# Kernel optimization log

Hardware: AMD Instinct MI355X
Metric: run time of the kernel (lower is better)

## Reference

```python
import jax, jax.numpy as jnp
import numpy as np

D = 256            # voxel grid resolution per axis
B, H, N = 1, 480 * 640, 9   # batch, pixels, samples per ray


def setup_inputs() -> dict:
    key = jax.random.key(0)
    k1, k2, k3 = jax.random.split(key, 3)
    # ray sample points in voxel coordinates; range slightly exceeds the grid
    # so the out-of-bounds masking path is exercised.
    points = jax.random.uniform(k1, (B, H, N, 3), dtype=jnp.float32,
                                minval=-2.0, maxval=float(D) + 1.0)
    tsdf_volume = jax.random.normal(k2, (D, D, D), dtype=jnp.float32)
    weights_volume = jax.random.uniform(k3, (D, D, D), dtype=jnp.float32)
    return {"points": points, "tsdf_volume": tsdf_volume,
            "weights_volume": weights_volume}


# binary corner offsets in the same (i, j, k) loop order as the original
_OFFS = np.array([[(c >> 2) & 1, (c >> 1) & 1, c & 1] for c in range(8)],
                 dtype=np.float32)  # [8, 3]


def _trilinear(points, tsdf_volume, weights_volume):
    b, h, n, _ = points.shape
    p = points.reshape(-1, 3)                      # [M, 3]
    idx = jnp.floor(p)
    center = idx + 0.5                             # mode='center'
    neighbor = jnp.sign(center - p)                # +-1 (0 exactly at center)
    alpha = jnp.abs(p - center)                    # [M, 3]
    alpha_inv = 1.0 - alpha
    offs = jnp.asarray(_OFFS, dtype=p.dtype)       # [8, 3]
    # per-corner trilinear weight: prod over dims of (alpha_inv if off==0 else alpha)
    w = jnp.prod(jnp.where(offs[None] == 0,
                           alpha_inv[:, None, :], alpha[:, None, :]),
                 axis=-1)                          # [M, 8]
    corner = idx[:, None, :] + offs[None] * neighbor[:, None, :]  # [M, 8, 3]
    ci = corner.astype(jnp.int32)
    dims = jnp.asarray(tsdf_volume.shape, dtype=jnp.int32)
    valid = jnp.all((ci >= 0) & (ci < dims[None, None, :]), axis=-1)  # [M, 8]
    cc = jnp.clip(ci, 0, dims[None, None, :] - 1)
    vmask = valid.astype(p.dtype)
    tv = tsdf_volume[cc[..., 0], cc[..., 1], cc[..., 2]] * vmask      # [M, 8]
    wv = weights_volume[cc[..., 0], cc[..., 1], cc[..., 2]] * vmask   # [M, 8]
    fusion_values = jnp.sum(tv * w, axis=1).reshape(b, h, n)
    fusion_weights = jnp.sum(wv * w, axis=1).reshape(b, h, n)
    indices = ci.reshape(b, h, n, 8, 3)
    weights = w.reshape(b, h, n, 8)
    return fusion_values, indices, weights, fusion_weights


def reference(points, tsdf_volume, weights_volume):
    return _trilinear(points, tsdf_volume, weights_volume)
```

## Files before the change

### kernel.cpp

```cpp
#include <hip/hip_runtime.h>


typedef float v2f __attribute__((ext_vector_type(2)));
typedef float v4f __attribute__((ext_vector_type(4)));

__global__ __launch_bounds__(256) void pack_brick_kernel(
    const float* __restrict__ tsdf,
    const float* __restrict__ wvol,
    float* __restrict__ packed)
{
    const int t = blockIdx.x * 256 + threadIdx.x;
    const int bz = t & 127;
    const int by = (t >> 7) & 127;
    const int bx = t >> 14;
    const int x0 = bx << 1, y0 = by << 1, z0 = bz << 1;

    v4f o[4];
#pragma unroll
    for (int dx = 0; dx < 2; ++dx) {
#pragma unroll
        for (int dy = 0; dy < 2; ++dy) {
            const size_t src = ((size_t)(x0 + dx) << 16) |
                               (size_t)((y0 + dy) << 8) | (size_t)z0;
            const v2f tp = *reinterpret_cast<const v2f*>(tsdf + src);
            const v2f wp = *reinterpret_cast<const v2f*>(wvol + src);
            v4f o4; o4.x = tp.x; o4.y = wp.x; o4.z = tp.y; o4.w = wp.y;
            o[dx * 2 + dy] = o4;
        }
    }
    v4f* __restrict__ dst = reinterpret_cast<v4f*>(packed + ((size_t)t << 4));
    dst[0] = o[0];
    dst[1] = o[1];
    dst[2] = o[2];
    dst[3] = o[3];
}

__global__ __launch_bounds__(256) void extractor_packed(
    const float* __restrict__ points,
    const float* __restrict__ packed,
    float* __restrict__ out,
    int M)
{
    const int m = blockIdx.x * 256 + threadIdx.x;
    if (m >= M) return;

    const size_t p3 = 3ull * (size_t)m;
    const float px = points[p3 + 0];
    const float py = points[p3 + 1];
    const float pz = points[p3 + 2];

    const float fx = floorf(px), fy = floorf(py), fz = floorf(pz);
    const int bx = (int)fx, by = (int)fy, bz = (int)fz;

    const float dxc = fx + 0.5f - px;
    const float dyc = fy + 0.5f - py;
    const float dzc = fz + 0.5f - pz;

    const int nx = (dxc > 0.f) ? 1 : ((dxc < 0.f) ? -1 : 0);
    const int ny = (dyc > 0.f) ? 1 : ((dyc < 0.f) ? -1 : 0);
    const int nz = (dzc > 0.f) ? 1 : ((dzc < 0.f) ? -1 : 0);

    const float ax = fabsf(dxc), ay = fabsf(dyc), az = fabsf(dzc);
    const float axi = 1.f - ax, ayi = 1.f - ay, azi = 1.f - az;

    float fv = 0.f, fw = 0.f;
    float idxf[24];
    float wts[8];

#pragma unroll
    for (int c = 0; c < 8; ++c) {
        const int ox = (c >> 2) & 1;
        const int oy = (c >> 1) & 1;
        const int oz = c & 1;
        const int cx = bx + (ox ? nx : 0);
        const int cy = by + (oy ? ny : 0);
        const int cz = bz + (oz ? nz : 0);
        const float w = (ox ? ax : axi) * (oy ? ay : ayi) * (oz ? az : azi);
        const bool valid = ((unsigned)cx < 256u) & ((unsigned)cy < 256u) & ((unsigned)cz < 256u);
        const int ccx = min(max(cx, 0), 255);
        const int ccy = min(max(cy, 0), 255);
        const int ccz = min(max(cz, 0), 255);
        const int brick = ((ccx >> 1) << 14) | ((ccy >> 1) << 7) | (ccz >> 1);
        const int off = ((ccx & 1) << 2) | ((ccy & 1) << 1) | (ccz & 1);
        const size_t fidx = ((size_t)brick << 4) + (size_t)(off << 1);
        const float vm = valid ? 1.f : 0.f;
        const v2f tw = *reinterpret_cast<const v2f*>(packed + fidx);
        fv += tw.x * vm * w;
        fw += tw.y * vm * w;
        idxf[c * 3 + 0] = (float)cx;
        idxf[c * 3 + 1] = (float)cy;
        idxf[c * 3 + 2] = (float)cz;
        wts[c] = w;
    }

    const size_t Ms = (size_t)M;
    out[m] = fv;
    out[33 * Ms + m] = fw;

    float4* __restrict__ oi = reinterpret_cast<float4*>(out + Ms + (size_t)m * 24);
    const float4* ii = reinterpret_cast<const float4*>(idxf);
#pragma unroll
    for (int i = 0; i < 6; ++i) oi[i] = ii[i];

    float4* __restrict__ ow = reinterpret_cast<float4*>(out + 25 * Ms + (size_t)m * 8);
    const float4* wi = reinterpret_cast<const float4*>(wts);
    ow[0] = wi[0];
    ow[1] = wi[1];
}

__global__ __launch_bounds__(256) void extractor_kernel(
    const float* __restrict__ points,
    const float* __restrict__ tsdf,
    const float* __restrict__ wvol,
    float* __restrict__ out,
    int M)
{
    const int m = blockIdx.x * 256 + threadIdx.x;
    if (m >= M) return;

    const size_t p3 = 3ull * (size_t)m;
    const float px = points[p3 + 0];
    const float py = points[p3 + 1];
    const float pz = points[p3 + 2];

    const float fx = floorf(px), fy = floorf(py), fz = floorf(pz);
    const int bx = (int)fx, by = (int)fy, bz = (int)fz;

    const float dxc = fx + 0.5f - px;
    const float dyc = fy + 0.5f - py;
    const float dzc = fz + 0.5f - pz;

    const int nx = (dxc > 0.f) ? 1 : ((dxc < 0.f) ? -1 : 0);
    const int ny = (dyc > 0.f) ? 1 : ((dyc < 0.f) ? -1 : 0);
    const int nz = (dzc > 0.f) ? 1 : ((dzc < 0.f) ? -1 : 0);

    const float ax = fabsf(dxc), ay = fabsf(dyc), az = fabsf(dzc);
    const float axi = 1.f - ax, ayi = 1.f - ay, azi = 1.f - az;

    float fv = 0.f, fw = 0.f;
    float idxf[24];
    float wts[8];

#pragma unroll
    for (int c = 0; c < 8; ++c) {
        const int ox = (c >> 2) & 1;
        const int oy = (c >> 1) & 1;
        const int oz = c & 1;
        const int cx = bx + (ox ? nx : 0);
        const int cy = by + (oy ? ny : 0);
        const int cz = bz + (oz ? nz : 0);
        const float w = (ox ? ax : axi) * (oy ? ay : ayi) * (oz ? az : azi);
        const bool valid = ((unsigned)cx < 256u) & ((unsigned)cy < 256u) & ((unsigned)cz < 256u);
        const int ccx = min(max(cx, 0), 255);
        const int ccy = min(max(cy, 0), 255);
        const int ccz = min(max(cz, 0), 255);
        const int flat = (ccx << 16) | (ccy << 8) | ccz;
        const float vm = valid ? 1.f : 0.f;
        const float tv = tsdf[flat] * vm;
        const float wv = wvol[flat] * vm;
        fv += tv * w;
        fw += wv * w;
        idxf[c * 3 + 0] = (float)cx;
        idxf[c * 3 + 1] = (float)cy;
        idxf[c * 3 + 2] = (float)cz;
        wts[c] = w;
    }

    const size_t Ms = (size_t)M;
    out[m] = fv;
    out[33 * Ms + m] = fw;

    float4* __restrict__ oi = reinterpret_cast<float4*>(out + Ms + (size_t)m * 24);
    const float4* ii = reinterpret_cast<const float4*>(idxf);
#pragma unroll
    for (int i = 0; i < 6; ++i) oi[i] = ii[i];

    float4* __restrict__ ow = reinterpret_cast<float4*>(out + 25 * Ms + (size_t)m * 8);
    const float4* wi = reinterpret_cast<const float4*>(wts);
    ow[0] = wi[0];
    ow[1] = wi[1];
}

extern "C" void kernel_launch(void* const* d_in, const int* in_sizes, int n_in,
                              void* d_out, int out_size, void* d_ws, size_t ws_size,
                              hipStream_t stream) {
    const float* points = (const float*)d_in[0];
    const float* tsdf   = (const float*)d_in[1];
    const float* wvol   = (const float*)d_in[2];
    float* out = (float*)d_out;

    const int M = in_sizes[0] / 3;
    const int blocks = (M + 255) / 256;

    const size_t nvox = 256ull * 256ull * 256ull;
    const size_t needed = nvox * 2ull * sizeof(float);

    if (ws_size >= needed) {
        float* packed = (float*)d_ws;
        const int nbricks = 128 * 128 * 128;
        pack_brick_kernel<<<nbricks / 256, 256, 0, stream>>>(tsdf, wvol, packed);
        extractor_packed<<<blocks, 256, 0, stream>>>(points, packed, out, M);
    } else {
        extractor_kernel<<<blocks, 256, 0, stream>>>(points, tsdf, wvol, out, M);
    }
}
```

Measured before the change: 705.1 us.

## Add z-duplicated packed volume layout so each xy corner pair loads as one float4

Adds a packing kernel that stores, for every 2x2 xy brick and every z, the tsdf and weight values at z and z+1 interleaved, which doubles the packed buffer to 256 MB. The extractor then takes both z corners for each xy pair with a single 16-byte load and selects between them, cutting gathers from 8 to 4 per point. In exchange the pack step reads and writes twice as much memory, and the path is used only when the workspace is large enough.

```diff
diff --git a/kernel.cpp b/kernel.cpp
--- a/kernel.cpp
+++ b/kernel.cpp
@@ -3,6 +3,135 @@
 
 typedef float v2f __attribute__((ext_vector_type(2)));
 typedef float v4f __attribute__((ext_vector_type(4)));
+
+__global__ __launch_bounds__(256) void pack_zdup_kernel(
+    const float* __restrict__ tsdf,
+    const float* __restrict__ wvol,
+    float* __restrict__ packed)
+{
+    const int t = blockIdx.x * 256 + threadIdx.x;
+    const int z  = t & 255;
+    const int brick = t >> 8;
+    const int y0 = (brick & 127) << 1;
+    const int x0 = (brick >> 7) << 1;
+    const int z1 = min(z + 1, 255);
+
+    float* __restrict__ dst = packed + ((size_t)t << 4);
+#pragma unroll
+    for (int dx = 0; dx < 2; ++dx) {
+#pragma unroll
+        for (int dy = 0; dy < 2; ++dy) {
+            const size_t base = ((size_t)(x0 + dx) << 16) |
+                                ((size_t)(y0 + dy) << 8);
+            v4f e;
+            e.x = tsdf[base + z];
+            e.y = wvol[base + z];
+            e.z = tsdf[base + z1];
+            e.w = wvol[base + z1];
+            *reinterpret_cast<v4f*>(dst + ((dx * 2 + dy) << 2)) = e;
+        }
+    }
+}
+
+__global__ __launch_bounds__(256) void extractor_zdup(
+    const float* __restrict__ points,
+    const float* __restrict__ packed,
+    float* __restrict__ out,
+    int M)
+{
+    const int m = blockIdx.x * 256 + threadIdx.x;
+    if (m >= M) return;
+
+    const size_t p3 = 3ull * (size_t)m;
+    const float px = points[p3 + 0];
+    const float py = points[p3 + 1];
+    const float pz = points[p3 + 2];
+
+    const float fx = floorf(px), fy = floorf(py), fz = floorf(pz);
+    const int bx = (int)fx, by = (int)fy, bz = (int)fz;
+
+    const float dxc = fx + 0.5f - px;
+    const float dyc = fy + 0.5f - py;
+    const float dzc = fz + 0.5f - pz;
+
+    const int nx = (dxc > 0.f) ? 1 : ((dxc < 0.f) ? -1 : 0);
+    const int ny = (dyc > 0.f) ? 1 : ((dyc < 0.f) ? -1 : 0);
+    const int nz = (dzc > 0.f) ? 1 : ((dzc < 0.f) ? -1 : 0);
+
+    const float ax = fabsf(dxc), ay = fabsf(dyc), az = fabsf(dzc);
+    const float axi = 1.f - ax, ayi = 1.f - ay, azi = 1.f - az;
+
+    const int cz0 = bz;
+    const int cz1 = bz + nz;
+    const int zlo = min(max(bz + min(nz, 0), 0), 254);
+    const int ccz0 = min(max(cz0, 0), 255);
+    const int ccz1 = min(max(cz1, 0), 255);
+    const int sel0 = ccz0 - zlo;
+    const int sel1 = ccz1 - zlo;
+    const bool vz0 = ((unsigned)cz0 < 256u);
+    const bool vz1 = ((unsigned)cz1 < 256u);
+
+    float fv = 0.f, fw = 0.f;
+    float idxf[24];
+    float wts[8];
+
+#pragma unroll
+    for (int q = 0; q < 4; ++q) {
+        const int ox = q >> 1;
+        const int oy = q & 1;
+        const int cx = bx + (ox ? nx : 0);
+        const int cy = by + (oy ? ny : 0);
+        const bool vxy = ((unsigned)cx < 256u) & ((unsigned)cy < 256u);
+        const int ccx = min(max(cx, 0), 255);
+        const int ccy = min(max(cy, 0), 255);
+        const float wxy = (ox ? ax : axi) * (oy ? ay : ayi);
+
+        const int entry = (((((ccx >> 1) << 7) | (ccy >> 1)) << 8 | zlo) << 2)
+                        | (((ccx & 1) << 1) | (ccy & 1));
+        const v4f qv = *reinterpret_cast<const v4f*>(packed + ((size_t)entry << 2));
+
+        {
+            const float t  = sel0 ? qv.z : qv.x;
+            const float wv = sel0 ? qv.w : qv.y;
+            const float vm = (vxy & vz0) ? 1.f : 0.f;
+            const float w  = wxy * azi;
+            fv += (t * vm) * w;
+            fw += (wv * vm) * w;
+            const int c = 2 * q;
+            idxf[c * 3 + 0] = (float)cx;
+            idxf[c * 3 + 1] = (float)cy;
+            idxf[c * 3 + 2] = (float)cz0;
+            wts[c] = w;
+        }
+        {
+            const float t  = sel1 ? qv.z : qv.x;
+            const float wv = sel1 ? qv.w : qv.y;
+            const float vm = (vxy & vz1) ? 1.f : 0.f;
+            const float w  = wxy * az;
+            fv += (t * vm) * w;
+            fw += (wv * vm) * w;
+            const int c = 2 * q + 1;
+            idxf[c * 3 + 0] = (float)cx;
+            idxf[c * 3 + 1] = (float)cy;
+            idxf[c * 3 + 2] = (float)cz1;
+            wts[c] = w;
+        }
+    }
+
+    const size_t Ms = (size_t)M;
+    out[m] = fv;
+    out[33 * Ms + m] = fw;
+
+    float4* __restrict__ oi = reinterpret_cast<float4*>(out + Ms + (size_t)m * 24);
+    const float4* ii = reinterpret_cast<const float4*>(idxf);
+#pragma unroll
+    for (int i = 0; i < 6; ++i) oi[i] = ii[i];
+
+    float4* __restrict__ ow = reinterpret_cast<float4*>(out + 25 * Ms + (size_t)m * 8);
+    const float4* wi = reinterpret_cast<const float4*>(wts);
+    ow[0] = wi[0];
+    ow[1] = wi[1];
+}
 
 __global__ __launch_bounds__(256) void pack_brick_kernel(
     const float* __restrict__ tsdf,
@@ -192,10 +321,15 @@
     const int M = in_sizes[0] / 3;
     const int blocks = (M + 255) / 256;
 
-    const size_t nvox = 256ull * 256ull * 256ull;
-    const size_t needed = nvox * 2ull * sizeof(float);
-
-    if (ws_size >= needed) {
+    const size_t need_zdup  = 268435456ull;
+    const size_t need_brick = 134217728ull;
+
+    if (ws_size >= need_zdup) {
+        float* packed = (float*)d_ws;
+        const int nthreads = 16384 * 256;
+        pack_zdup_kernel<<<nthreads / 256, 256, 0, stream>>>(tsdf, wvol, packed);
+        extractor_zdup<<<blocks, 256, 0, stream>>>(points, packed, out, M);
+    } else if (ws_size >= need_brick) {
         float* packed = (float*)d_ws;
         const int nbricks = 128 * 128 * 128;
         pack_brick_kernel<<<nbricks / 256, 256, 0, stream>>>(tsdf, wvol, packed);
```

New measurement: 745.2 us. +5.7%, slower.
